# Kernel optimization log

Hardware: AMD Instinct MI355X
Metric: run time of the kernel (lower is better)

## Reference

```python
import jax, jax.numpy as jnp
import numpy as np

D_IN, D_SAE, T, L, K = 2304, 2048, 4, 6, 128
B = 32


def setup_inputs() -> dict:
    key = jax.random.key(0)
    kx, ke, kd = jax.random.split(key, 3)
    x = jax.random.normal(kx, (B, T, L, D_IN), dtype=jnp.float32)
    W_enc = jax.random.normal(ke, (T, L, D_IN, D_SAE), dtype=jnp.float32) / np.sqrt(D_IN).astype(np.float32)
    W_dec = jax.random.normal(kd, (T, L, D_SAE, D_IN), dtype=jnp.float32) / np.sqrt(D_SAE).astype(np.float32)
    b_enc = jnp.zeros((D_SAE,), dtype=jnp.float32)
    b_dec = jnp.zeros((T, L, D_IN), dtype=jnp.float32)
    return {"x": x, "W_enc": W_enc, "W_dec": W_dec, "b_enc": b_enc, "b_dec": b_dec}


def reference(x, W_enc, W_dec, b_enc, b_dec):
    # encode: per-(t,l) matmul, pre: (B, T, L, d_sae)
    pre = jnp.einsum('btld,tlds->btls', x, W_enc) + b_enc
    Bn = pre.shape[0]
    pre_flat = pre.reshape(Bn, T * L * D_SAE)
    # global TopK over the whole (T, L, d_sae) latent grid
    v, idx = jax.lax.top_k(pre_flat, K)
    z_flat = jnp.zeros_like(pre_flat).at[jnp.arange(Bn)[:, None], idx].set(jax.nn.relu(v))
    z = z_flat.reshape(Bn, T, L, D_SAE)
    # decode: per-(t,l) matmul
    x_hat = jnp.einsum('btls,tlsd->btld', z, W_dec) + b_dec
    loss = jnp.mean(jnp.sum(jnp.square(x_hat - x), axis=-1))
    return (loss, x_hat, z)
```

## Files before the change

### kernel.cpp

```cpp
#include <hip/hip_runtime.h>

#define D_IN   2304
#define D_SAE  2048
#define TL     24
#define BATCH  32
#define K_TOP  128
#define NLAT   (TL * D_SAE)
#define NBIN   8192
#define CAP    2048
#define KSPLIT 2
#define KS     (D_IN / KSPLIT)
#define BK     32
#define NCH    (KS / BK)
#define TOPK_T 512

typedef __attribute__((ext_vector_type(8))) short short8;
typedef __attribute__((ext_vector_type(4))) float f32x4;

__device__ __forceinline__ void async_cp16(const float* g, float* l) {
    __builtin_amdgcn_global_load_lds(
        (const __attribute__((address_space(1))) unsigned int*)g,
        (__attribute__((address_space(3))) unsigned int*)l, 16, 0, 0);
}

__device__ __forceinline__ void cvt8(const float* f, short8& hi, short8& lo) {
#pragma unroll
    for (int j = 0; j < 8; ++j) {
        unsigned u = __float_as_uint(f[j]);
        hi[j] = (short)(u >> 16);
        float l = f[j] - __uint_as_float(u & 0xFFFF0000u);
        lo[j] = (short)(__float_as_uint(l) >> 16);
    }
}
__device__ __forceinline__ void cvt44(float4 a, float4 b, short8& hi, short8& lo) {
    float f[8];
    *(float4*)&f[0] = a; *(float4*)&f[4] = b;
    cvt8(f, hi, lo);
}

__global__ __launch_bounds__(256, 3) void enc_kernel(const float* __restrict__ x,
                                                     const float* __restrict__ W,
                                                     float* __restrict__ part) {
    __shared__ float w_s[3][BK][128];

    const int tid  = threadIdx.x;
    const int lane = tid & 63;
    const int wv   = tid >> 6;
    const int m0   = lane & 15;
    const int kb   = lane >> 4;
    const int tl   = blockIdx.y;
    const int ks   = blockIdx.z;
    const int col0 = blockIdx.x * 128;

    const float* Wbase = W + ((size_t)(tl * D_IN + ks * KS)) * D_SAE + col0;
    const float* xsrc0 = x + ((size_t)(m0 * TL + tl)) * D_IN + ks * KS + kb * 8;
    const float* xsrc1 = x + ((size_t)((16 + m0) * TL + tl)) * D_IN + ks * KS + kb * 8;

    float4 xr0[4], xr1[4], xr2[4];

#define STAGE(BUF, CH)                                                          \
    do {                                                                        \
        const float* Wc = Wbase + (size_t)(CH) * BK * D_SAE;                    \
        _Pragma("unroll")                                                       \
        for (int i = 0; i < 4; ++i)                                             \
            async_cp16(Wc + (size_t)(wv * 8 + 2 * i + (lane >> 5)) * D_SAE      \
                          + (lane & 31) * 4,                                    \
                       &w_s[BUF][wv * 8 + 2 * i][0]);                           \
        xr##BUF[0] = *(const float4*)(xsrc0 + (CH) * BK);                       \
        xr##BUF[1] = *(const float4*)(xsrc0 + (CH) * BK + 4);                   \
        xr##BUF[2] = *(const float4*)(xsrc1 + (CH) * BK);                       \
        xr##BUF[3] = *(const float4*)(xsrc1 + (CH) * BK + 4);                   \
    } while (0)

    f32x4 acc[2][2];
#pragma unroll
    for (int mt = 0; mt < 2; ++mt)
#pragma unroll
        for (int nt = 0; nt < 2; ++nt) acc[mt][nt] = (f32x4)(0.f);

#define COMPUTE(BUF)                                                            \
    do {                                                                        \
        const float(*ws)[128] = w_s[BUF];                                       \
        short8 a0h, a0l, a1h, a1l;                                              \
        cvt44(xr##BUF[0], xr##BUF[1], a0h, a0l);                                \
        cvt44(xr##BUF[2], xr##BUF[3], a1h, a1l);                                \
        _Pragma("unroll")                                                       \
        for (int nt = 0; nt < 2; ++nt) {                                        \
            float wf[8];                                                        \
            _Pragma("unroll")                                                   \
            for (int j = 0; j < 8; ++j)                                         \
                wf[j] = ws[kb * 8 + j][wv * 32 + nt * 16 + m0];                 \
            short8 bhi, blo;                                                    \
            cvt8(wf, bhi, blo);                                                 \
            acc[0][nt] = __builtin_amdgcn_mfma_f32_16x16x32_bf16(a0h, bhi, acc[0][nt], 0, 0, 0); \
            acc[0][nt] = __builtin_amdgcn_mfma_f32_16x16x32_bf16(a0h, blo, acc[0][nt], 0, 0, 0); \
            acc[0][nt] = __builtin_amdgcn_mfma_f32_16x16x32_bf16(a0l, bhi, acc[0][nt], 0, 0, 0); \
            acc[1][nt] = __builtin_amdgcn_mfma_f32_16x16x32_bf16(a1h, bhi, acc[1][nt], 0, 0, 0); \
            acc[1][nt] = __builtin_amdgcn_mfma_f32_16x16x32_bf16(a1h, blo, acc[1][nt], 0, 0, 0); \
            acc[1][nt] = __builtin_amdgcn_mfma_f32_16x16x32_bf16(a1l, bhi, acc[1][nt], 0, 0, 0); \
        }                                                                       \
    } while (0)

#define ITER(BUF, NXT, C)                                                       \
    do {                                                                        \
        if ((C) + 1 < NCH) { asm volatile("s_waitcnt vmcnt(8)" ::: "memory"); } \
        else               { asm volatile("s_waitcnt vmcnt(0)" ::: "memory"); } \
        __builtin_amdgcn_s_barrier();                                           \
        if ((C) + 2 < NCH) STAGE(NXT, (C) + 2);                                 \
        COMPUTE(BUF);                                                           \
    } while (0)

    STAGE(0, 0);
    STAGE(1, 1);
    for (int c3 = 0; c3 < NCH; c3 += 3) {
        ITER(0, 2, c3);
        ITER(1, 0, c3 + 1);
        ITER(2, 1, c3 + 2);
    }
#undef ITER
#undef COMPUTE
#undef STAGE

    float* pp = part + ((size_t)ks * BATCH) * NLAT + (size_t)tl * D_SAE + col0;
#pragma unroll
    for (int mt = 0; mt < 2; ++mt)
#pragma unroll
        for (int nt = 0; nt < 2; ++nt)
#pragma unroll
            for (int r = 0; r < 4; ++r)
                pp[(size_t)(mt * 16 + kb * 4 + r) * NLAT + wv * 32 + nt * 16 + m0] =
                    acc[mt][nt][r];
}

__global__ void reduce_kernel(const float* __restrict__ part,
                              const float* __restrict__ b_enc,
                              float* __restrict__ pre,
                              float* __restrict__ z,
                              float* __restrict__ loss) {
    int i = (blockIdx.x * blockDim.x + threadIdx.x) * 4;
    const size_t S = (size_t)BATCH * NLAT;
    float4 v = *(const float4*)&b_enc[i & (D_SAE - 1)];
#pragma unroll
    for (int s = 0; s < KSPLIT; s++) {
        float4 p = *(const float4*)&part[i + s * S];
        v.x += p.x; v.y += p.y; v.z += p.z; v.w += p.w;
    }
    *(float4*)&pre[i] = v;
    z[i] = 0.f; z[i + 1] = 0.f; z[i + 2] = 0.f; z[i + 3] = 0.f;
    if (i == 0) *loss = 0.f;
}

__global__ __launch_bounds__(TOPK_T) void topk_kernel(const float* __restrict__ pre,
                                                      int* __restrict__ sel_idx,
                                                      float* __restrict__ sel_val,
                                                      float* __restrict__ z) {
    const int b   = blockIdx.x;
    const int tid = threadIdx.x;
    __shared__ unsigned hist[NBIN];
    __shared__ unsigned cand_key[CAP];
    __shared__ int      cand_idx[CAP];
    __shared__ unsigned tsum[TOPK_T];
    __shared__ unsigned scan[TOPK_T];
    __shared__ int s_T, s_hi, s_ccnt, s_sel;

    const float* row  = pre + (size_t)b * NLAT;
    float*       zrow = z   + (size_t)b * NLAT;
    for (int i = tid; i < NBIN; i += TOPK_T) hist[i] = 0;
    if (tid == 0) { s_ccnt = 0; s_sel = 0; }
    __syncthreads();

    for (int i = 4 * tid; i < NLAT; i += 4 * TOPK_T) {
        float4 v = *(const float4*)&row[i];
#pragma unroll
        for (int j = 0; j < 4; j++) {
            unsigned u   = __float_as_uint(((const float*)&v)[j]);
            unsigned key = u ^ ((u >> 31) ? 0xFFFFFFFFu : 0x80000000u);
            atomicAdd(&hist[key >> 19], 1u);
        }
    }
    __syncthreads();

    unsigned local = 0;
    const int base = tid * (NBIN / TOPK_T);
#pragma unroll
    for (int j = 0; j < NBIN / TOPK_T; j++) local += hist[base + j];
    tsum[tid] = local;
    scan[tid] = local;
    __syncthreads();
    for (int d = 1; d < TOPK_T; d <<= 1) {
        unsigned v = scan[tid] + ((tid + d < TOPK_T) ? scan[tid + d] : 0u);
        __syncthreads();
        scan[tid] = v;
        __syncthreads();
    }
    const unsigned suf_e = scan[tid] - tsum[tid];
    if (suf_e < K_TOP && suf_e + tsum[tid] >= K_TOP) {
        unsigned c = suf_e;
        for (int j = NBIN / TOPK_T - 1; j >= 0; j--) {
            int bin = base + j;
            if (c + hist[bin] >= K_TOP) { s_T = bin; s_hi = (int)c; break; }
            c += hist[bin];
        }
    }
    __syncthreads();

    const int T = s_T;
    for (int i = 4 * tid; i < NLAT; i += 4 * TOPK_T) {
        float4 v = *(const float4*)&row[i];
#pragma unroll
        for (int j = 0; j < 4; j++) {
            float f      = ((const float*)&v)[j];
            unsigned u   = __float_as_uint(f);
            unsigned key = u ^ ((u >> 31) ? 0xFFFFFFFFu : 0x80000000u);
            int bin      = (int)(key >> 19);
            if (bin > T) {
                int p = atomicAdd(&s_sel, 1);
                float rl = fmaxf(f, 0.f);
                sel_idx[b * K_TOP + p] = i + j;
                sel_val[b * K_TOP + p] = rl;
                zrow[i + j] = rl;
            } else if (bin == T) {
                int p = atomicAdd(&s_ccnt, 1);
                if (p < CAP) { cand_key[p] = key; cand_idx[p] = i + j; }
            }
        }
    }
    __syncthreads();

    const int need = K_TOP - s_hi;
    const int nc   = min(s_ccnt, CAP);
    for (int c = tid; c < nc; c += TOPK_T) {
        unsigned kc = cand_key[c]; int ic = cand_idx[c];
        int rank = 0;
        for (int j = 0; j < nc; j++) {
            unsigned kj = cand_key[j]; int ij = cand_idx[j];
            rank += (kj > kc) || (kj == kc && ij < ic);
        }
        if (rank < need) {
            int p = atomicAdd(&s_sel, 1);
            float rl = fmaxf(row[ic], 0.f);
            sel_idx[b * K_TOP + p] = ic;
            sel_val[b * K_TOP + p] = rl;
            zrow[ic] = rl;
        }
    }
}

__global__ __launch_bounds__(256) void dec_kernel(const float* __restrict__ Wd,
                                                  const float* __restrict__ b_dec,
                                                  const float* __restrict__ x,
                                                  const int* __restrict__ sel_idx,
                                                  const float* __restrict__ sel_val,
                                                  float* __restrict__ xhat,
                                                  float* __restrict__ loss) {
    const int tl = blockIdx.x, b = blockIdx.y, tid = threadIdx.x;
    float acc[9];
#pragma unroll
    for (int r = 0; r < 9; r++) acc[r] = b_dec[tl * D_IN + tid + r * 256];

    __shared__ int   s_idx[K_TOP];
    __shared__ float s_val[K_TOP];
    if (tid < K_TOP) { s_idx[tid] = sel_idx[b * K_TOP + tid];
                       s_val[tid] = sel_val[b * K_TOP + tid]; }
    __syncthreads();

    for (int j = 0; j < K_TOP; j++) {
        int f = s_idx[j];
        if ((f >> 11) == tl) {
            float v = s_val[j];
            const float* wrow = Wd + (size_t)f * D_IN;
#pragma unroll
            for (int r = 0; r < 9; r++)
                acc[r] = fmaf(v, wrow[tid + r * 256], acc[r]);
        }
    }

    const float* xr = x    + ((size_t)b * TL + tl) * D_IN;
    float*       xo = xhat + ((size_t)b * TL + tl) * D_IN;
    float lsum = 0.f;
#pragma unroll
    for (int r = 0; r < 9; r++) {
        float d = acc[r] - xr[tid + r * 256];
        xo[tid + r * 256] = acc[r];
        lsum += d * d;
    }
    __shared__ float red[256];
    red[tid] = lsum; __syncthreads();
    for (int s = 128; s > 0; s >>= 1) {
        if (tid < s) red[tid] += red[tid + s];
        __syncthreads();
    }
    if (tid == 0) atomicAdd(loss, red[0] * (1.0f / (BATCH * TL)));
}

extern "C" void kernel_launch(void* const* d_in, const int* in_sizes, int n_in,
                              void* d_out, int out_size, void* d_ws, size_t ws_size,
                              hipStream_t stream) {
    const float* x     = (const float*)d_in[0];
    const float* W_enc = (const float*)d_in[1];
    const float* W_dec = (const float*)d_in[2];
    const float* b_enc = (const float*)d_in[3];
    const float* b_dec = (const float*)d_in[4];

    float* out  = (float*)d_out;
    float* loss = out;
    float* xhat = out + 1;
    float* z    = out + 1 + (size_t)BATCH * TL * D_IN;

    const size_t S = (size_t)BATCH * NLAT;
    float* part    = (float*)d_ws;
    float* pre     = part + (size_t)KSPLIT * S;
    int*   sel_idx = (int*)(pre + S);
    float* sel_val = (float*)(sel_idx + BATCH * K_TOP);

    enc_kernel<<<dim3(16, TL, KSPLIT), 256, 0, stream>>>(x, W_enc, part);
    reduce_kernel<<<(int)(S / 1024), 256, 0, stream>>>(part, b_enc, pre, z, loss);
    topk_kernel<<<BATCH, TOPK_T, 0, stream>>>(pre, sel_idx, sel_val, z);
    dec_kernel<<<dim3(TL, BATCH), 256, 0, stream>>>(W_dec, b_dec, x, sel_idx, sel_val,
                                                    xhat, loss);
}
```

Before: 158.3 us.

## Load encoder weights directly into registers instead of async LDS staging

The encoder GEMM stops staging W tiles through shared memory with async global-to-LDS copies and barriers. Each lane now loads its own W column elements straight from global memory into registers, with a two-deep register double buffer, and occupancy is lowered to 2 blocks per SM to fit the extra registers. This removes LDS traffic and block barriers. In exchange, the W loads become scalar, strided by row and less coalesced (16 lanes per contiguous segment), and fewer warps are available to hide latency.

```diff
diff --git a/kernel.cpp b/kernel.cpp
--- a/kernel.cpp
+++ b/kernel.cpp
@@ -17,12 +17,6 @@
 typedef __attribute__((ext_vector_type(8))) short short8;
 typedef __attribute__((ext_vector_type(4))) float f32x4;
 
-__device__ __forceinline__ void async_cp16(const float* g, float* l) {
-    __builtin_amdgcn_global_load_lds(
-        (const __attribute__((address_space(1))) unsigned int*)g,
-        (__attribute__((address_space(3))) unsigned int*)l, 16, 0, 0);
-}
-
 __device__ __forceinline__ void cvt8(const float* f, short8& hi, short8& lo) {
 #pragma unroll
     for (int j = 0; j < 8; ++j) {
@@ -38,11 +32,9 @@
     cvt8(f, hi, lo);
 }
 
-__global__ __launch_bounds__(256, 3) void enc_kernel(const float* __restrict__ x,
+__global__ __launch_bounds__(256, 2) void enc_kernel(const float* __restrict__ x,
                                                      const float* __restrict__ W,
                                                      float* __restrict__ part) {
-    __shared__ float w_s[3][BK][128];
-
     const int tid  = threadIdx.x;
     const int lane = tid & 63;
     const int wv   = tid >> 6;
@@ -52,24 +44,26 @@
     const int ks   = blockIdx.z;
     const int col0 = blockIdx.x * 128;
 
-    const float* Wbase = W + ((size_t)(tl * D_IN + ks * KS)) * D_SAE + col0;
+    const float* Wl = W + ((size_t)(tl * D_IN + ks * KS) + kb * 8) * D_SAE
+                    + col0 + wv * 32 + m0;
     const float* xsrc0 = x + ((size_t)(m0 * TL + tl)) * D_IN + ks * KS + kb * 8;
     const float* xsrc1 = x + ((size_t)((16 + m0) * TL + tl)) * D_IN + ks * KS + kb * 8;
 
-    float4 xr0[4], xr1[4], xr2[4];
-
-#define STAGE(BUF, CH)                                                          \
+    float  wA[16], wB[16];
+    float4 xA[4],  xB[4];
+
+#define LOADG(S, CH)                                                            \
     do {                                                                        \
-        const float* Wc = Wbase + (size_t)(CH) * BK * D_SAE;                    \
+        const float* Wc = Wl + (size_t)(CH) * BK * D_SAE;                       \
         _Pragma("unroll")                                                       \
-        for (int i = 0; i < 4; ++i)                                             \
-            async_cp16(Wc + (size_t)(wv * 8 + 2 * i + (lane >> 5)) * D_SAE      \
-                          + (lane & 31) * 4,                                    \
-                       &w_s[BUF][wv * 8 + 2 * i][0]);                           \
-        xr##BUF[0] = *(const float4*)(xsrc0 + (CH) * BK);                       \
-        xr##BUF[1] = *(const float4*)(xsrc0 + (CH) * BK + 4);                   \
-        xr##BUF[2] = *(const float4*)(xsrc1 + (CH) * BK);                       \
-        xr##BUF[3] = *(const float4*)(xsrc1 + (CH) * BK + 4);                   \
+        for (int j = 0; j < 8; ++j) {                                           \
+            w##S[j]     = Wc[(size_t)j * D_SAE];                                \
+            w##S[8 + j] = Wc[(size_t)j * D_SAE + 16];                           \
+        }                                                                       \
+        x##S[0] = *(const float4*)(xsrc0 + (CH) * BK);                          \
+        x##S[1] = *(const float4*)(xsrc0 + (CH) * BK + 4);                      \
+        x##S[2] = *(const float4*)(xsrc1 + (CH) * BK);                          \
+        x##S[3] = *(const float4*)(xsrc1 + (CH) * BK + 4);                      \
     } while (0)
 
     f32x4 acc[2][2];
@@ -78,48 +72,37 @@
 #pragma unroll
         for (int nt = 0; nt < 2; ++nt) acc[mt][nt] = (f32x4)(0.f);
 
-#define COMPUTE(BUF)                                                            \
+#define COMPUTE(S)                                                              \
     do {                                                                        \
-        const float(*ws)[128] = w_s[BUF];                                       \
-        short8 a0h, a0l, a1h, a1l;                                              \
-        cvt44(xr##BUF[0], xr##BUF[1], a0h, a0l);                                \
-        cvt44(xr##BUF[2], xr##BUF[3], a1h, a1l);                                \
-        _Pragma("unroll")                                                       \
-        for (int nt = 0; nt < 2; ++nt) {                                        \
-            float wf[8];                                                        \
-            _Pragma("unroll")                                                   \
-            for (int j = 0; j < 8; ++j)                                         \
-                wf[j] = ws[kb * 8 + j][wv * 32 + nt * 16 + m0];                 \
-            short8 bhi, blo;                                                    \
-            cvt8(wf, bhi, blo);                                                 \
-            acc[0][nt] = __builtin_amdgcn_mfma_f32_16x16x32_bf16(a0h, bhi, acc[0][nt], 0, 0, 0); \
-            acc[0][nt] = __builtin_amdgcn_mfma_f32_16x16x32_bf16(a0h, blo, acc[0][nt], 0, 0, 0); \
-            acc[0][nt] = __builtin_amdgcn_mfma_f32_16x16x32_bf16(a0l, bhi, acc[0][nt], 0, 0, 0); \
-            acc[1][nt] = __builtin_amdgcn_mfma_f32_16x16x32_bf16(a1h, bhi, acc[1][nt], 0, 0, 0); \
-            acc[1][nt] = __builtin_amdgcn_mfma_f32_16x16x32_bf16(a1h, blo, acc[1][nt], 0, 0, 0); \
-            acc[1][nt] = __builtin_amdgcn_mfma_f32_16x16x32_bf16(a1l, bhi, acc[1][nt], 0, 0, 0); \
-        }                                                                       \
+        short8 a0h, a0l, a1h, a1l, b0h, b0l, b1h, b1l;                          \
+        cvt44(x##S[0], x##S[1], a0h, a0l);                                      \
+        cvt44(x##S[2], x##S[3], a1h, a1l);                                      \
+        cvt8(&w##S[0], b0h, b0l);                                               \
+        cvt8(&w##S[8], b1h, b1l);                                               \
+        acc[0][0] = __builtin_amdgcn_mfma_f32_16x16x32_bf16(a0h, b0h, acc[0][0], 0, 0, 0); \
+        acc[0][0] = __builtin_amdgcn_mfma_f32_16x16x32_bf16(a0h, b0l, acc[0][0], 0, 0, 0); \
+        acc[0][0] = __builtin_amdgcn_mfma_f32_16x16x32_bf16(a0l, b0h, acc[0][0], 0, 0, 0); \
+        acc[1][0] = __builtin_amdgcn_mfma_f32_16x16x32_bf16(a1h, b0h, acc[1][0], 0, 0, 0); \
+        acc[1][0] = __builtin_amdgcn_mfma_f32_16x16x32_bf16(a1h, b0l, acc[1][0], 0, 0, 0); \
+        acc[1][0] = __builtin_amdgcn_mfma_f32_16x16x32_bf16(a1l, b0h, acc[1][0], 0, 0, 0); \
+        acc[0][1] = __builtin_amdgcn_mfma_f32_16x16x32_bf16(a0h, b1h, acc[0][1], 0, 0, 0); \
+        acc[0][1] = __builtin_amdgcn_mfma_f32_16x16x32_bf16(a0h, b1l, acc[0][1], 0, 0, 0); \
+        acc[0][1] = __builtin_amdgcn_mfma_f32_16x16x32_bf16(a0l, b1h, acc[0][1], 0, 0, 0); \
+        acc[1][1] = __builtin_amdgcn_mfma_f32_16x16x32_bf16(a1h, b1h, acc[1][1], 0, 0, 0); \
+        acc[1][1] = __builtin_amdgcn_mfma_f32_16x16x32_bf16(a1h, b1l, acc[1][1], 0, 0, 0); \
+        acc[1][1] = __builtin_amdgcn_mfma_f32_16x16x32_bf16(a1l, b1h, acc[1][1], 0, 0, 0); \
     } while (0)
 
-#define ITER(BUF, NXT, C)                                                       \
-    do {                                                                        \
-        if ((C) + 1 < NCH) { asm volatile("s_waitcnt vmcnt(8)" ::: "memory"); } \
-        else               { asm volatile("s_waitcnt vmcnt(0)" ::: "memory"); } \
-        __builtin_amdgcn_s_barrier();                                           \
-        if ((C) + 2 < NCH) STAGE(NXT, (C) + 2);                                 \
-        COMPUTE(BUF);                                                           \
-    } while (0)
-
-    STAGE(0, 0);
-    STAGE(1, 1);
-    for (int c3 = 0; c3 < NCH; c3 += 3) {
-        ITER(0, 2, c3);
-        ITER(1, 0, c3 + 1);
-        ITER(2, 1, c3 + 2);
-    }
-#undef ITER
+    LOADG(A, 0);
+    LOADG(B, 1);
+    for (int ch = 0; ch < NCH; ch += 2) {
+        COMPUTE(A);
+        if (ch + 2 < NCH) LOADG(A, ch + 2);
+        COMPUTE(B);
+        if (ch + 3 < NCH) LOADG(B, ch + 3);
+    }
 #undef COMPUTE
-#undef STAGE
+#undef LOADG
 
     float* pp = part + ((size_t)ks * BATCH) * NLAT + (size_t)tl * D_SAE + col0;
 #pragma unroll
```

After: 161.9 us. 2.3% more time.

## Split per-row top-k into segmented histogram, threshold, select and tie kernels

Applied to the files above, without the earlier changes.

Replaces the single-block-per-row top-k kernel (32 blocks total) with four kernels: per-segment histograms across 8 blocks per row, a threshold scan per row, segmented selection with global atomics, and a small tie-break kernel. The aim is to spread the two full passes over each 49k-element row across many more workgroups instead of leaving most CUs idle. In exchange it adds three extra launches, a global histogram round trip and global atomics. It also lowers the candidate cap from 2048 to 512, which could drop tied candidates if a bin is crowded.

```diff
diff --git a/kernel.cpp b/kernel.cpp
--- a/kernel.cpp
+++ b/kernel.cpp
@@ -6,13 +6,14 @@
 #define BATCH  32
 #define K_TOP  128
 #define NLAT   (TL * D_SAE)
+#define NSEG   8
+#define SEGLEN (NLAT / NSEG)
 #define NBIN   8192
-#define CAP    2048
+#define CCAP   512
 #define KSPLIT 2
 #define KS     (D_IN / KSPLIT)
 #define BK     32
 #define NCH    (KS / BK)
-#define TOPK_T 512
 
 typedef __attribute__((ext_vector_type(8))) short short8;
 typedef __attribute__((ext_vector_type(4))) float f32x4;
@@ -150,45 +151,55 @@
     if (i == 0) *loss = 0.f;
 }
 
-__global__ __launch_bounds__(TOPK_T) void topk_kernel(const float* __restrict__ pre,
-                                                      int* __restrict__ sel_idx,
-                                                      float* __restrict__ sel_val,
-                                                      float* __restrict__ z) {
-    const int b   = blockIdx.x;
-    const int tid = threadIdx.x;
-    __shared__ unsigned hist[NBIN];
-    __shared__ unsigned cand_key[CAP];
-    __shared__ int      cand_idx[CAP];
-    __shared__ unsigned tsum[TOPK_T];
-    __shared__ unsigned scan[TOPK_T];
-    __shared__ int s_T, s_hi, s_ccnt, s_sel;
-
-    const float* row  = pre + (size_t)b * NLAT;
-    float*       zrow = z   + (size_t)b * NLAT;
-    for (int i = tid; i < NBIN; i += TOPK_T) hist[i] = 0;
-    if (tid == 0) { s_ccnt = 0; s_sel = 0; }
-    __syncthreads();
-
-    for (int i = 4 * tid; i < NLAT; i += 4 * TOPK_T) {
+__global__ __launch_bounds__(256) void hist8_kernel(const float* __restrict__ pre,
+                                                    unsigned* __restrict__ ghist,
+                                                    int* __restrict__ selcnt,
+                                                    int* __restrict__ candcnt) {
+    const int seg = blockIdx.x, b = blockIdx.y, tid = threadIdx.x;
+    __shared__ unsigned h[NBIN];
+    for (int i = tid; i < NBIN; i += 256) h[i] = 0;
+    if (seg == 0 && tid == 0) { selcnt[b] = 0; candcnt[b] = 0; }
+    __syncthreads();
+
+    const float* row = pre + (size_t)b * NLAT + seg * SEGLEN;
+    for (int i = 4 * tid; i < SEGLEN; i += 1024) {
         float4 v = *(const float4*)&row[i];
 #pragma unroll
         for (int j = 0; j < 4; j++) {
             unsigned u   = __float_as_uint(((const float*)&v)[j]);
             unsigned key = u ^ ((u >> 31) ? 0xFFFFFFFFu : 0x80000000u);
-            atomicAdd(&hist[key >> 19], 1u);
-        }
+            atomicAdd(&h[key >> 19], 1u);
+        }
+    }
+    __syncthreads();
+    unsigned* gh = ghist + (size_t)b * NBIN * NSEG;
+    for (int i = tid; i < NBIN; i += 256) gh[(size_t)i * NSEG + seg] = h[i];
+}
+
+__global__ __launch_bounds__(512) void thresh_kernel(const unsigned* __restrict__ ghist,
+                                                     int* __restrict__ Tb,
+                                                     int* __restrict__ hib) {
+    const int b = blockIdx.x, tid = threadIdx.x;
+    __shared__ unsigned hist[NBIN];
+    __shared__ unsigned tsum[512], scan[512];
+    __shared__ int sT, shi;
+    const unsigned* gh = ghist + (size_t)b * NBIN * NSEG;
+    for (int i = tid; i < NBIN; i += 512) {
+        uint4 a = *(const uint4*)&gh[(size_t)i * NSEG];
+        uint4 c = *(const uint4*)&gh[(size_t)i * NSEG + 4];
+        hist[i] = a.x + a.y + a.z + a.w + c.x + c.y + c.z + c.w;
     }
     __syncthreads();
 
     unsigned local = 0;
-    const int base = tid * (NBIN / TOPK_T);
-#pragma unroll
-    for (int j = 0; j < NBIN / TOPK_T; j++) local += hist[base + j];
+    const int base = tid * (NBIN / 512);
+#pragma unroll
+    for (int j = 0; j < NBIN / 512; j++) local += hist[base + j];
     tsum[tid] = local;
     scan[tid] = local;
     __syncthreads();
-    for (int d = 1; d < TOPK_T; d <<= 1) {
-        unsigned v = scan[tid] + ((tid + d < TOPK_T) ? scan[tid + d] : 0u);
+    for (int d = 1; d < 512; d <<= 1) {
+        unsigned v = scan[tid] + ((tid + d < 512) ? scan[tid + d] : 0u);
         __syncthreads();
         scan[tid] = v;
         __syncthreads();
@@ -196,52 +207,86 @@
     const unsigned suf_e = scan[tid] - tsum[tid];
     if (suf_e < K_TOP && suf_e + tsum[tid] >= K_TOP) {
         unsigned c = suf_e;
-        for (int j = NBIN / TOPK_T - 1; j >= 0; j--) {
+        for (int j = NBIN / 512 - 1; j >= 0; j--) {
             int bin = base + j;
-            if (c + hist[bin] >= K_TOP) { s_T = bin; s_hi = (int)c; break; }
+            if (c + hist[bin] >= K_TOP) { sT = bin; shi = (int)c; break; }
             c += hist[bin];
         }
     }
     __syncthreads();
-
-    const int T = s_T;
-    for (int i = 4 * tid; i < NLAT; i += 4 * TOPK_T) {
+    if (tid == 0) { Tb[b] = sT; hib[b] = shi; }
+}
+
+__global__ __launch_bounds__(256) void select_kernel(const float* __restrict__ pre,
+                                                     const int* __restrict__ Tb,
+                                                     int* __restrict__ selcnt,
+                                                     int* __restrict__ sel_idx,
+                                                     float* __restrict__ sel_val,
+                                                     int* __restrict__ candcnt,
+                                                     unsigned* __restrict__ cand_key,
+                                                     int* __restrict__ cand_idx,
+                                                     float* __restrict__ cand_val,
+                                                     float* __restrict__ z) {
+    const int seg = blockIdx.x, b = blockIdx.y;
+    const int T = Tb[b];
+    const float* row  = pre + (size_t)b * NLAT;
+    float*       zrow = z   + (size_t)b * NLAT;
+    for (int i = seg * SEGLEN + threadIdx.x * 4; i < (seg + 1) * SEGLEN; i += 1024) {
         float4 v = *(const float4*)&row[i];
 #pragma unroll
-        for (int j = 0; j < 4; j++) {
+        for (int j = 0; j < 4; ++j) {
             float f      = ((const float*)&v)[j];
             unsigned u   = __float_as_uint(f);
             unsigned key = u ^ ((u >> 31) ? 0xFFFFFFFFu : 0x80000000u);
             int bin      = (int)(key >> 19);
             if (bin > T) {
-                int p = atomicAdd(&s_sel, 1);
+                int p = atomicAdd(&selcnt[b], 1);
                 float rl = fmaxf(f, 0.f);
                 sel_idx[b * K_TOP + p] = i + j;
                 sel_val[b * K_TOP + p] = rl;
                 zrow[i + j] = rl;
             } else if (bin == T) {
-                int p = atomicAdd(&s_ccnt, 1);
-                if (p < CAP) { cand_key[p] = key; cand_idx[p] = i + j; }
+                int q = atomicAdd(&candcnt[b], 1);
+                if (q < CCAP) {
+                    cand_key[b * CCAP + q] = key;
+                    cand_idx[b * CCAP + q] = i + j;
+                    cand_val[b * CCAP + q] = f;
+                }
             }
         }
     }
-    __syncthreads();
-
-    const int need = K_TOP - s_hi;
-    const int nc   = min(s_ccnt, CAP);
-    for (int c = tid; c < nc; c += TOPK_T) {
-        unsigned kc = cand_key[c]; int ic = cand_idx[c];
+}
+
+__global__ __launch_bounds__(64) void tie_kernel(const int* __restrict__ hib,
+                                                 const int* __restrict__ candcnt,
+                                                 const unsigned* __restrict__ cand_key,
+                                                 const int* __restrict__ cand_idx,
+                                                 const float* __restrict__ cand_val,
+                                                 int* __restrict__ sel_idx,
+                                                 float* __restrict__ sel_val,
+                                                 float* __restrict__ z) {
+    const int b = blockIdx.x, tid = threadIdx.x;
+    const int nc = min(candcnt[b], CCAP);
+    const int hi = hib[b], need = K_TOP - hi;
+    __shared__ unsigned k_s[CCAP];
+    __shared__ int      i_s[CCAP];
+    __shared__ float    v_s[CCAP];
+    for (int c = tid; c < nc; c += 64) {
+        k_s[c] = cand_key[b * CCAP + c];
+        i_s[c] = cand_idx[b * CCAP + c];
+        v_s[c] = cand_val[b * CCAP + c];
+    }
+    __syncthreads();
+    for (int c = tid; c < nc; c += 64) {
+        unsigned kc = k_s[c]; int ic = i_s[c];
         int rank = 0;
-        for (int j = 0; j < nc; j++) {
-            unsigned kj = cand_key[j]; int ij = cand_idx[j];
-            rank += (kj > kc) || (kj == kc && ij < ic);
-        }
+        for (int j = 0; j < nc; ++j)
+            rank += (k_s[j] > kc) || (k_s[j] == kc && i_s[j] < ic);
         if (rank < need) {
-            int p = atomicAdd(&s_sel, 1);
-            float rl = fmaxf(row[ic], 0.f);
-            sel_idx[b * K_TOP + p] = ic;
-            sel_val[b * K_TOP + p] = rl;
-            zrow[ic] = rl;
+            float rl = fmaxf(v_s[c], 0.f);
+            sel_idx[b * K_TOP + hi + rank] = ic;
+            sel_val[b * K_TOP + hi + rank] = rl;
+            z[(size_t)b * NLAT + ic] = rl;
         }
     }
 }
@@ -308,14 +353,28 @@
     float* z    = out + 1 + (size_t)BATCH * TL * D_IN;
 
     const size_t S = (size_t)BATCH * NLAT;
-    float* part    = (float*)d_ws;
-    float* pre     = part + (size_t)KSPLIT * S;
-    int*   sel_idx = (int*)(pre + S);
-    float* sel_val = (float*)(sel_idx + BATCH * K_TOP);
+    float*    part     = (float*)d_ws;
+    float*    pre      = part + (size_t)KSPLIT * S;
+    unsigned* ghist    = (unsigned*)(pre + S);
+    int*      Tb       = (int*)(ghist + (size_t)BATCH * NBIN * NSEG);
+    int*      hib      = Tb + BATCH;
+    int*      selcnt   = hib + BATCH;
+    int*      candcnt  = selcnt + BATCH;
+    int*      sel_idx  = candcnt + BATCH;
+    float*    sel_val  = (float*)(sel_idx + BATCH * K_TOP);
+    unsigned* cand_key = (unsigned*)(sel_val + BATCH * K_TOP);
+    int*      cand_idx = (int*)(cand_key + BATCH * CCAP);
+    float*    cand_val = (float*)(cand_idx + BATCH * CCAP);
 
     enc_kernel<<<dim3(16, TL, KSPLIT), 256, 0, stream>>>(x, W_enc, part);
     reduce_kernel<<<(int)(S / 1024), 256, 0, stream>>>(part, b_enc, pre, z, loss);
-    topk_kernel<<<BATCH, TOPK_T, 0, stream>>>(pre, sel_idx, sel_val, z);
+    hist8_kernel<<<dim3(NSEG, BATCH), 256, 0, stream>>>(pre, ghist, selcnt, candcnt);
+    thresh_kernel<<<BATCH, 512, 0, stream>>>(ghist, Tb, hib);
+    select_kernel<<<dim3(NSEG, BATCH), 256, 0, stream>>>(pre, Tb, selcnt, sel_idx,
+                                                         sel_val, candcnt, cand_key,
+                                                         cand_idx, cand_val, z);
+    tie_kernel<<<BATCH, 64, 0, stream>>>(hib, candcnt, cand_key, cand_idx, cand_val,
+                                         sel_idx, sel_val, z);
     dec_kernel<<<dim3(TL, BATCH), 256, 0, stream>>>(W_dec, b_dec, x, sel_idx, sel_val,
                                                     xhat, loss);
 }
```

New measurement: 197.0 us. 1.24x slower.
